# Optimization experiments

Hardware: AMD Instinct MI355X
Metric: run time of the kernel (lower is better)

Reference implementation:

```python
import jax, jax.numpy as jnp
import numpy as np

DIM = 192
HEADS = 6
HD = DIM // HEADS            # 32
RES = (32, 64, 64)           # D, H, W
WS = (4, 4, 4)               # window size
NW_TOK = WS[0] * WS[1] * WS[2]   # 64 tokens per window
L = RES[0] * RES[1] * RES[2]     # 131072
HIDDEN = 4 * DIM
B = 2


def _rel_pos_index():
    # faithful to the torch buffer construction (3D branch)
    coords = np.stack(np.meshgrid(*[np.arange(w) for w in WS], indexing='ij'))  # (3, wd, wh, ww)
    cf = coords.reshape(3, -1)                     # (3, 64)
    rel = cf[:, :, None] - cf[:, None, :]          # (3, 64, 64)
    rel = rel.transpose(1, 2, 0).astype(np.int64)  # (64, 64, 3)
    for i in range(3):
        rel[:, :, i] += WS[i] - 1
    rel[:, :, 0] *= (2 * WS[1] - 1) * (2 * WS[2] - 1)
    rel[:, :, 1] *= 2 * WS[2] - 1
    return rel.sum(-1)                             # (64, 64)


def setup_inputs() -> dict:
    key = jax.random.key(0)
    ks = jax.random.split(key, 8)
    s = 0.02
    d = {}
    d['skip'] = jax.random.normal(ks[0], (B, L, DIM), jnp.float32)
    d['x_up'] = jax.random.normal(ks[1], (B, L, DIM), jnp.float32)
    # norms
    d['g1'] = jnp.ones((DIM,), jnp.float32); d['be1'] = jnp.zeros((DIM,), jnp.float32)
    d['g2'] = jnp.ones((DIM,), jnp.float32); d['be2'] = jnp.zeros((DIM,), jnp.float32)
    # attention params
    d['Wkv'] = jax.random.normal(ks[2], (DIM, 2 * DIM), jnp.float32) * s
    d['bkv'] = jnp.zeros((2 * DIM,), jnp.float32)
    d['Wproj'] = jax.random.normal(ks[3], (DIM, DIM), jnp.float32) * s
    d['bproj'] = jnp.zeros((DIM,), jnp.float32)
    d['bias_table'] = jax.random.normal(ks[4], ((2 * WS[0] - 1) * (2 * WS[1] - 1) * (2 * WS[2] - 1), HEADS), jnp.float32) * s
    d['rel_idx'] = jnp.asarray(_rel_pos_index(), jnp.int32)
    # MLP params
    d['W1'] = jax.random.normal(ks[5], (DIM, HIDDEN), jnp.float32) * s
    d['b1'] = jnp.zeros((HIDDEN,), jnp.float32)
    d['W2'] = jax.random.normal(ks[6], (HIDDEN, DIM), jnp.float32) * s
    d['b2'] = jnp.zeros((DIM,), jnp.float32)
    return d


def _ln(x, g, b):
    mu = x.mean(-1, keepdims=True)
    var = x.var(-1, keepdims=True)
    return (x - mu) * jax.lax.rsqrt(var + 1e-5) * g + b


def _win_part(x):
    # x: (B, D, H, W, C) -> (B*nW, 64, C)
    D, H, W = RES; wd, wh, ww = WS
    x = x.reshape(B, D // wd, wd, H // wh, wh, W // ww, ww, DIM)
    x = x.transpose(0, 1, 3, 5, 2, 4, 6, 7)
    return x.reshape(-1, NW_TOK, DIM)


def _win_rev(w):
    # (B*nW, 64, C) -> (B, L, C)
    D, H, W = RES; wd, wh, ww = WS
    x = w.reshape(B, D // wd, H // wh, W // ww, wd, wh, ww, DIM)
    x = x.transpose(0, 1, 4, 2, 5, 3, 6, 7)
    return x.reshape(B, L, DIM)


def reference(skip, x_up, g1, be1, g2, be2, Wkv, bkv, Wproj, bproj,
              bias_table, rel_idx, W1, b1, W2, b2):
    shortcut = skip
    s = _ln(skip, g1, be1).reshape(B, *RES, DIM)
    u = _ln(x_up, g1, be1).reshape(B, *RES, DIM)
    sw = _win_part(s)   # kv source: (Bw, 64, C)
    uw = _win_part(u)   # q source
    Bw = sw.shape[0]
    kv = (sw @ Wkv + bkv).reshape(Bw, NW_TOK, 2, HEADS, HD)
    k = kv[:, :, 0].transpose(0, 2, 1, 3)   # (Bw, h, 64, hd)
    v = kv[:, :, 1].transpose(0, 2, 1, 3)
    q = uw.reshape(Bw, NW_TOK, HEADS, HD).transpose(0, 2, 1, 3)
    scale = HD ** -0.5
    attn = jnp.einsum('bhqd,bhkd->bhqk', q * scale, k)
    bias = bias_table[rel_idx.reshape(-1)].reshape(NW_TOK, NW_TOK, HEADS).transpose(2, 0, 1)
    attn = jax.nn.softmax(attn + bias[None], axis=-1)
    o = jnp.einsum('bhqk,bhkd->bhqd', attn, v).transpose(0, 2, 1, 3).reshape(Bw, NW_TOK, DIM)
    o = o @ Wproj + bproj
    x = shortcut + _win_rev(o)
    h = _ln(x, g2, be2)
    h = jax.nn.gelu(h @ W1 + b1, approximate=False)
    return x + (h @ W2 + b2)
```

## Files before the change

kernel.cpp:

```cpp
#include <hip/hip_runtime.h>
#include <hip/hip_bf16.h>

typedef __hip_bfloat16 bf16;
typedef short s8v __attribute__((ext_vector_type(8)));
typedef float f32x4 __attribute__((ext_vector_type(4)));

__device__ __forceinline__ float b2f(bf16 v) { return __bfloat162float(v); }
__device__ __forceinline__ bf16 f2b(float v) { return __float2bfloat16(v); }

union H8 { bf16 h[8]; s8v v; uint2 u2[2]; };

__device__ __forceinline__ float gelu_f(float v) {
    float z = fabsf(v) * 0.70710678118654752f;
    float t = 1.f / (1.f + 0.3275911f * z);
    float poly = t * (0.254829592f + t * (-0.284496736f + t * (1.421413741f +
                 t * (-1.453152027f + t * 1.061405429f))));
    float erfz = 1.f - poly * __expf(-z * z);
    erfz = copysignf(erfz, v);
    return 0.5f * v * (1.f + erfz);
}

__device__ __forceinline__ void stage_frag(const bf16* __restrict__ img, bf16* lds,
                                           int nseg, int wv, int lane) {
    for (int seg = wv; seg < nseg; seg += 4) {
        __builtin_amdgcn_global_load_lds(
            (const __attribute__((address_space(1))) void*)(img + seg * 512 + (lane << 3)),
            (__attribute__((address_space(3))) void*)(lds + seg * 512),
            16, 0, 0);
    }
}

__global__ __launch_bounds__(256) void k_prep(
    const float* __restrict__ Wkv, const float* __restrict__ Wproj,
    const float* __restrict__ W1,  const float* __restrict__ W2,
    bf16* __restrict__ ws)
{
    int t = blockIdx.x * 256 + threadIdx.x;
    if (t >= 50688) return;
    int k, n, ld;
    const float* W;
    bf16* dst;
    if (t < 9216) {
        int c = t / 1152, r = t % 1152;
        int tile = r >> 6, lane = r & 63;
        int ks = tile / 3, nt = tile % 3;
        n = c * 48 + nt * 16 + (lane & 15);
        k = ks * 32 + (lane >> 4) * 8;
        W = Wkv; ld = 384; dst = ws + t * 8;
    } else if (t < 13824) {
        int t2 = t - 9216;
        int c = t2 / 1152, r = t2 % 1152;
        int tile = r >> 6, lane = r & 63;
        int ks = tile / 3, nt = tile % 3;
        n = c * 48 + nt * 16 + (lane & 15);
        k = ks * 32 + (lane >> 4) * 8;
        W = Wproj; ld = 192; dst = ws + 73728 + t2 * 8;
    } else {
        int t3 = t - 13824;
        int c = t3 / 1536, r = t3 % 1536;
        int half = r / 768, rr = r % 768;
        int tile = rr >> 6, lane = rr & 63;
        int lr = lane & 15, g = lane >> 4;
        if (half == 0) {
            int ks = tile >> 1, nt2 = tile & 1;
            n = c * 32 + nt2 * 16 + lr; k = ks * 32 + g * 8; W = W1; ld = 768;
        } else {
            n = tile * 16 + lr; k = c * 32 + g * 8; W = W2; ld = 192;
        }
        dst = ws + 110592 + t3 * 8;
    }
    #pragma unroll
    for (int e = 0; e < 8; ++e) dst[e] = f2b(W[(k + e) * ld + n]);
}

__global__ __launch_bounds__(256, 2) void k_attn(
    const float* __restrict__ skip, const float* __restrict__ xup,
    const float* __restrict__ g1,   const float* __restrict__ be1,
    const bf16*  __restrict__ imgKv,const float* __restrict__ bkv,
    const bf16*  __restrict__ imgPr,const float* __restrict__ bproj,
    const float* __restrict__ btab, const int*  __restrict__ relidx,
    float* __restrict__ xout)
{
    __shared__ __align__(16) bf16 sK[64 * 200];
    __shared__ __align__(16) char poolRaw[36864];
    __shared__ __align__(1024) bf16 sWt[9216];

    bf16* sVt = (bf16*)poolRaw;
    bf16* sP  = (bf16*)(poolRaw + 27648);
    bf16* sO  = (bf16*)poolRaw;

    const int tid = threadIdx.x;
    const int lane = tid & 63;
    const int wv = tid >> 6;
    const int g = lane >> 4;
    const int lr = lane & 15;
    const int w = blockIdx.x;
    const int b = w >> 11;
    const int widx = w & 2047;
    const int d0 = widx >> 8, h0 = (widx >> 4) & 15, w0 = widx & 15;

    #define GROW(t) (b * 131072 + (d0 * 4 + ((t) >> 4)) * 4096 + \
                     (h0 * 4 + (((t) >> 2) & 3)) * 64 + (w0 * 4 + ((t) & 3)))

    const int myrow = wv * 16 + lr;
    const int growA = GROW(myrow) * 192;
    float4 u4[12], s4[12];
    #pragma unroll
    for (int ks = 0; ks < 6; ++ks) {
        int k0 = 32 * ks + 8 * g;
        u4[2 * ks]     = *(const float4*)(xup  + growA + k0);
        u4[2 * ks + 1] = *(const float4*)(xup  + growA + k0 + 4);
        s4[2 * ks]     = *(const float4*)(skip + growA + k0);
        s4[2 * ks + 1] = *(const float4*)(skip + growA + k0 + 4);
    }
    float su = 0, squ = 0, ss = 0, sqs = 0;
    #pragma unroll
    for (int i = 0; i < 12; ++i) {
        const float* up = &u4[i].x;
        const float* sp = &s4[i].x;
        #pragma unroll
        for (int e = 0; e < 4; ++e) {
            su += up[e]; squ += up[e] * up[e];
            ss += sp[e]; sqs += sp[e] * sp[e];
        }
    }
    su += __shfl_xor(su, 16);  su += __shfl_xor(su, 32);
    squ += __shfl_xor(squ, 16); squ += __shfl_xor(squ, 32);
    ss += __shfl_xor(ss, 16);  ss += __shfl_xor(ss, 32);
    sqs += __shfl_xor(sqs, 16); sqs += __shfl_xor(sqs, 32);
    const float inv192 = 1.f / 192.f;
    float muU = su * inv192, vU = squ * inv192 - muU * muU;
    float muS = ss * inv192, vS = sqs * inv192 - muS * muS;
    float rU = rsqrtf(vU + 1e-5f), rS = rsqrtf(vS + 1e-5f);
    const float scale = 0.17677669529663687f;

    s8v qreg[6], sreg[6];
    #pragma unroll
    for (int ks = 0; ks < 6; ++ks) {
        H8 qa, sa;
        #pragma unroll
        for (int half = 0; half < 2; ++half) {
            const float* up = &u4[2 * ks + half].x;
            const float* sp = &s4[2 * ks + half].x;
            #pragma unroll
            for (int e = 0; e < 4; ++e) {
                int k = 32 * ks + 8 * g + 4 * half + e;
                float gg = g1[k], bb = be1[k];
                qa.h[4 * half + e] = f2b(((up[e] - muU) * rU * gg + bb) * scale);
                sa.h[4 * half + e] = f2b((sp[e] - muS) * rS * gg + bb);
            }
        }
        qreg[ks] = qa.v; sreg[ks] = sa.v;
    }

    for (int nc = 0; nc < 8; ++nc) {
        __syncthreads();
        stage_frag(imgKv + nc * 9216, sWt, 18, wv, lane);
        __syncthreads();

        f32x4 acc[3];
        #pragma unroll
        for (int nt = 0; nt < 3; ++nt) acc[nt] = (f32x4){0.f, 0.f, 0.f, 0.f};
        #pragma unroll
        for (int ks = 0; ks < 6; ++ks) {
            #pragma unroll
            for (int nt = 0; nt < 3; ++nt) {
                s8v bfr = *(const s8v*)(sWt + ((ks * 3 + nt) * 64 + lane) * 8);
                acc[nt] = __builtin_amdgcn_mfma_f32_16x16x32_bf16(sreg[ks], bfr, acc[nt], 0, 0, 0);
            }
        }
        if (nc < 4) {
            #pragma unroll
            for (int nt = 0; nt < 3; ++nt) {
                int c = nc * 48 + nt * 16 + lr;
                float bias = bkv[c];
                #pragma unroll
                for (int e = 0; e < 4; ++e)
                    sK[(wv * 16 + 4 * g + e) * 200 + c] = f2b(acc[nt][e] + bias);
            }
        } else {
            #pragma unroll
            for (int nt = 0; nt < 3; ++nt) {
                int c = nc * 48 + nt * 16 + lr;
                float bias = bkv[c];
                int d = c - 192;
                H8 t4;
                #pragma unroll
                for (int e = 0; e < 4; ++e) t4.h[e] = f2b(acc[nt][e] + bias);
                *(uint2*)(sVt + d * 72 + wv * 16 + 4 * g) = t4.u2[0];
            }
        }
    }
    __syncthreads();

    int bidx[4][4];
    #pragma unroll
    for (int nt = 0; nt < 4; ++nt)
        #pragma unroll
        for (int e = 0; e < 4; ++e)
            bidx[nt][e] = relidx[(wv * 16 + 4 * g + e) * 64 + nt * 16 + lr] * 6;

    f32x4 accO[6][2];
    #pragma unroll
    for (int h = 0; h < 6; ++h)
        #pragma unroll
        for (int nt = 0; nt < 2; ++nt) accO[h][nt] = (f32x4){0.f, 0.f, 0.f, 0.f};

    #pragma unroll
    for (int h = 0; h < 6; ++h) {
        f32x4 s[4];
        #pragma unroll
        for (int nt = 0; nt < 4; ++nt) {
            s8v kf = *(const s8v*)(sK + (nt * 16 + lr) * 200 + h * 32 + 8 * g);
            s[nt] = __builtin_amdgcn_mfma_f32_16x16x32_bf16(qreg[h], kf,
                        (f32x4){0.f, 0.f, 0.f, 0.f}, 0, 0, 0);
        }
        #pragma unroll
        for (int nt = 0; nt < 4; ++nt)
            #pragma unroll
            for (int e = 0; e < 4; ++e)
                s[nt][e] += btab[bidx[nt][e] + h];
        float mx0 = fmaxf(fmaxf(s[0][0], s[1][0]), fmaxf(s[2][0], s[3][0]));
        float mx1 = fmaxf(fmaxf(s[0][1], s[1][1]), fmaxf(s[2][1], s[3][1]));
        float mx2 = fmaxf(fmaxf(s[0][2], s[1][2]), fmaxf(s[2][2], s[3][2]));
        float mx3 = fmaxf(fmaxf(s[0][3], s[1][3]), fmaxf(s[2][3], s[3][3]));
        #pragma unroll
        for (int m = 1; m <= 8; m <<= 1) {
            mx0 = fmaxf(mx0, __shfl_xor(mx0, m));
            mx1 = fmaxf(mx1, __shfl_xor(mx1, m));
            mx2 = fmaxf(mx2, __shfl_xor(mx2, m));
            mx3 = fmaxf(mx3, __shfl_xor(mx3, m));
        }
        float sm0 = 0, sm1 = 0, sm2 = 0, sm3 = 0;
        #pragma unroll
        for (int nt = 0; nt < 4; ++nt) {
            s[nt][0] = __expf(s[nt][0] - mx0); sm0 += s[nt][0];
            s[nt][1] = __expf(s[nt][1] - mx1); sm1 += s[nt][1];
            s[nt][2] = __expf(s[nt][2] - mx2); sm2 += s[nt][2];
            s[nt][3] = __expf(s[nt][3] - mx3); sm3 += s[nt][3];
        }
        #pragma unroll
        for (int m = 1; m <= 8; m <<= 1) {
            sm0 += __shfl_xor(sm0, m); sm1 += __shfl_xor(sm1, m);
            sm2 += __shfl_xor(sm2, m); sm3 += __shfl_xor(sm3, m);
        }
        float iv0 = 1.f / sm0, iv1 = 1.f / sm1, iv2 = 1.f / sm2, iv3 = 1.f / sm3;

        __syncthreads();
        #pragma unroll
        for (int nt = 0; nt < 4; ++nt) {
            int kt = nt * 16 + lr;
            sP[(wv * 16 + 4 * g + 0) * 72 + kt] = f2b(s[nt][0] * iv0);
            sP[(wv * 16 + 4 * g + 1) * 72 + kt] = f2b(s[nt][1] * iv1);
            sP[(wv * 16 + 4 * g + 2) * 72 + kt] = f2b(s[nt][2] * iv2);
            sP[(wv * 16 + 4 * g + 3) * 72 + kt] = f2b(s[nt][3] * iv3);
        }
        __syncthreads();

        s8v aP0 = *(const s8v*)(sP + (wv * 16 + lr) * 72 + 8 * g);
        s8v aP1 = *(const s8v*)(sP + (wv * 16 + lr) * 72 + 32 + 8 * g);
        #pragma unroll
        for (int nt = 0; nt < 2; ++nt) {
            const bf16* vb = sVt + (h * 32 + nt * 16 + lr) * 72;
            s8v v0 = *(const s8v*)(vb + 8 * g);
            s8v v1 = *(const s8v*)(vb + 32 + 8 * g);
            accO[h][nt] = __builtin_amdgcn_mfma_f32_16x16x32_bf16(aP0, v0, accO[h][nt], 0, 0, 0);
            accO[h][nt] = __builtin_amdgcn_mfma_f32_16x16x32_bf16(aP1, v1, accO[h][nt], 0, 0, 0);
        }
    }

    __syncthreads();
    #pragma unroll
    for (int h = 0; h < 6; ++h)
        #pragma unroll
        for (int nt = 0; nt < 2; ++nt) {
            int c = h * 32 + nt * 16 + lr;
            #pragma unroll
            for (int e = 0; e < 4; ++e)
                sO[(wv * 16 + 4 * g + e) * 200 + c] = f2b(accO[h][nt][e]);
        }
    __syncthreads();
    s8v aO[6];
    #pragma unroll
    for (int ks = 0; ks < 6; ++ks)
        aO[ks] = *(const s8v*)(sO + (wv * 16 + lr) * 200 + 32 * ks + 8 * g);

    int gq[4];
    #pragma unroll
    for (int e = 0; e < 4; ++e) gq[e] = GROW(wv * 16 + 4 * g + e) * 192;

    for (int nc = 0; nc < 4; ++nc) {
        __syncthreads();
        stage_frag(imgPr + nc * 9216, sWt, 18, wv, lane);
        __syncthreads();

        f32x4 acc[3];
        #pragma unroll
        for (int nt = 0; nt < 3; ++nt) acc[nt] = (f32x4){0.f, 0.f, 0.f, 0.f};
        #pragma unroll
        for (int ks = 0; ks < 6; ++ks) {
            #pragma unroll
            for (int nt = 0; nt < 3; ++nt) {
                s8v bfr = *(const s8v*)(sWt + ((ks * 3 + nt) * 64 + lane) * 8);
                acc[nt] = __builtin_amdgcn_mfma_f32_16x16x32_bf16(aO[ks], bfr, acc[nt], 0, 0, 0);
            }
        }
        #pragma unroll
        for (int nt = 0; nt < 3; ++nt) {
            int c = nc * 48 + nt * 16 + lr;
            float bp = bproj[c];
            #pragma unroll
            for (int e = 0; e < 4; ++e) {
                int go = gq[e] + c;
                xout[go] = acc[nt][e] + bp + skip[go];
            }
        }
    }
    #undef GROW
}

__global__ __launch_bounds__(256, 2) void k_mlp(
    float* __restrict__ xio,
    const float* __restrict__ g2, const float* __restrict__ be2,
    const bf16*  __restrict__ imgMlp,
    const float* __restrict__ b1, const float* __restrict__ b2)
{
    __shared__ __align__(1024) bf16 sW[2][12288];
    __shared__ __align__(16) bf16 sH[128 * 40];

    const int tid = threadIdx.x;
    const int lane = tid & 63;
    const int wv = tid >> 6;
    const int g = lane >> 4;
    const int lr = lane & 15;
    const int rowbase = blockIdx.x * 128;

    stage_frag(imgMlp, sW[0], 24, wv, lane);

    s8v xreg[2][6];
    #pragma unroll
    for (int mi = 0; mi < 2; ++mi) {
        const int row = rowbase + wv * 16 + mi * 64 + lr;
        float4 xa[12];
        #pragma unroll
        for (int ks = 0; ks < 6; ++ks) {
            int k0 = 32 * ks + 8 * g;
            xa[2 * ks]     = *(const float4*)(xio + row * 192 + k0);
            xa[2 * ks + 1] = *(const float4*)(xio + row * 192 + k0 + 4);
        }
        float s = 0, sq = 0;
        #pragma unroll
        for (int i = 0; i < 12; ++i) {
            const float* p = &xa[i].x;
            #pragma unroll
            for (int e = 0; e < 4; ++e) { s += p[e]; sq += p[e] * p[e]; }
        }
        s += __shfl_xor(s, 16);  s += __shfl_xor(s, 32);
        sq += __shfl_xor(sq, 16); sq += __shfl_xor(sq, 32);
        float mu = s * (1.f / 192.f), var = sq * (1.f / 192.f) - mu * mu;
        float rs = rsqrtf(var + 1e-5f);
        #pragma unroll
        for (int ks = 0; ks < 6; ++ks) {
            H8 xa8;
            #pragma unroll
            for (int half = 0; half < 2; ++half) {
                int k0 = 32 * ks + 8 * g + 4 * half;
                float4 gg = *(const float4*)(g2 + k0);
                float4 be = *(const float4*)(be2 + k0);
                const float* p = &xa[2 * ks + half].x;
                const float* gp = &gg.x;
                const float* bp = &be.x;
                #pragma unroll
                for (int e = 0; e < 4; ++e)
                    xa8.h[4 * half + e] = f2b((p[e] - mu) * rs * gp[e] + bp[e]);
            }
            xreg[mi][ks] = xa8.v;
        }
    }

    f32x4 accC[2][12];
    #pragma unroll
    for (int mi = 0; mi < 2; ++mi)
        #pragma unroll
        for (int nt = 0; nt < 12; ++nt) accC[mi][nt] = (f32x4){0.f, 0.f, 0.f, 0.f};

    for (int ch = 0; ch < 24; ++ch) {
        const int c = ch & 1;
        __syncthreads();
        if (ch < 23) stage_frag(imgMlp + (ch + 1) * 12288, sW[c ^ 1], 24, wv, lane);
        const bf16* wc = sW[c];

        f32x4 accH[2][2];
        #pragma unroll
        for (int mi = 0; mi < 2; ++mi)
            #pragma unroll
            for (int nt = 0; nt < 2; ++nt) accH[mi][nt] = (f32x4){0.f, 0.f, 0.f, 0.f};
        #pragma unroll
        for (int ks = 0; ks < 6; ++ks) {
            s8v b0  = *(const s8v*)(wc + ((ks * 2 + 0) * 64 + lane) * 8);
            s8v b1f = *(const s8v*)(wc + ((ks * 2 + 1) * 64 + lane) * 8);
            accH[0][0] = __builtin_amdgcn_mfma_f32_16x16x32_bf16(xreg[0][ks], b0,  accH[0][0], 0, 0, 0);
            accH[0][1] = __builtin_amdgcn_mfma_f32_16x16x32_bf16(xreg[0][ks], b1f, accH[0][1], 0, 0, 0);
            accH[1][0] = __builtin_amdgcn_mfma_f32_16x16x32_bf16(xreg[1][ks], b0,  accH[1][0], 0, 0, 0);
            accH[1][1] = __builtin_amdgcn_mfma_f32_16x16x32_bf16(xreg[1][ks], b1f, accH[1][1], 0, 0, 0);
        }

        #pragma unroll
        for (int mi = 0; mi < 2; ++mi)
            #pragma unroll
            for (int nt = 0; nt < 2; ++nt) {
                float bb = b1[ch * 32 + nt * 16 + lr];
                #pragma unroll
                for (int e = 0; e < 4; ++e) {
                    int row = wv * 16 + mi * 64 + g * 4 + e;
                    sH[row * 40 + nt * 16 + lr] = f2b(gelu_f(accH[mi][nt][e] + bb));
                }
            }
        __syncthreads();

        s8v aH0 = *(const s8v*)(sH + (wv * 16 + lr) * 40 + g * 8);
        s8v aH1 = *(const s8v*)(sH + (wv * 16 + 64 + lr) * 40 + g * 8);
        #pragma unroll
        for (int nt = 0; nt < 12; ++nt) {
            s8v bW = *(const s8v*)(wc + 6144 + (nt * 64 + lane) * 8);
            accC[0][nt] = __builtin_amdgcn_mfma_f32_16x16x32_bf16(aH0, bW, accC[0][nt], 0, 0, 0);
            accC[1][nt] = __builtin_amdgcn_mfma_f32_16x16x32_bf16(aH1, bW, accC[1][nt], 0, 0, 0);
        }
    }

    #pragma unroll
    for (int mi = 0; mi < 2; ++mi)
        #pragma unroll
        for (int nt = 0; nt < 12; ++nt) {
            int col = nt * 16 + lr;
            float bb = b2[col];
            #pragma unroll
            for (int e = 0; e < 4; ++e) {
                int row = rowbase + wv * 16 + mi * 64 + g * 4 + e;
                float* p = xio + row * 192 + col;
                *p = accC[mi][nt][e] + bb + *p;
            }
        }
}

extern "C" void kernel_launch(void* const* d_in, const int* in_sizes, int n_in,
                              void* d_out, int out_size, void* d_ws, size_t ws_size,
                              hipStream_t stream) {
    const float* skip   = (const float*)d_in[0];
    const float* xup    = (const float*)d_in[1];
    const float* g1     = (const float*)d_in[2];
    const float* be1    = (const float*)d_in[3];
    const float* g2     = (const float*)d_in[4];
    const float* be2    = (const float*)d_in[5];
    const float* Wkv    = (const float*)d_in[6];
    const float* bkv    = (const float*)d_in[7];
    const float* Wproj  = (const float*)d_in[8];
    const float* bproj  = (const float*)d_in[9];
    const float* btab   = (const float*)d_in[10];
    const int*  relidx  = (const int*)d_in[11];
    const float* W1     = (const float*)d_in[12];
    const float* b1     = (const float*)d_in[13];
    const float* W2     = (const float*)d_in[14];
    const float* b2     = (const float*)d_in[15];
    float* xio = (float*)d_out;
    bf16* ws = (bf16*)d_ws;

    k_prep<<<198, 256, 0, stream>>>(Wkv, Wproj, W1, W2, ws);
    k_attn<<<4096, 256, 0, stream>>>(skip, xup, g1, be1, ws, bkv,
                                     ws + 73728, bproj, btab, relidx, xio);
    k_mlp<<<2048, 256, 0, stream>>>(xio, g2, be2, ws + 110592, b1, b2);
}
```

Baseline: 612.1 us.

## Transpose MFMA operands so each wave owns its rows and drop block barriers

Swaps the A/B operands of the QK^T, PV and MLP-up MFMAs so each lane holds a whole row's values for four columns. Softmax then reduces with two cross-lane shuffles instead of four-step trees, and P, O and H fragments are written to LDS as packed 8-byte stores into rows owned only by the writing wave. That removes several __syncthreads per head and per MLP chunk. It also stages the relative-position bias table into LDS instead of reading it from global memory per element, which risks reusing the weight buffer region and relies on the per-wave LDS ownership being correct.

```diff
diff --git a/kernel.cpp b/kernel.cpp
--- a/kernel.cpp
+++ b/kernel.cpp
@@ -88,6 +88,7 @@
     bf16* sVt = (bf16*)poolRaw;
     bf16* sP  = (bf16*)(poolRaw + 27648);
     bf16* sO  = (bf16*)poolRaw;
+    float* sBt = (float*)sWt;
 
     const int tid = threadIdx.x;
     const int lane = tid & 63;
@@ -193,18 +194,20 @@
     }
     __syncthreads();
 
+    for (int i = tid; i < 2058; i += 256) sBt[i] = btab[i];
     int bidx[4][4];
     #pragma unroll
     for (int nt = 0; nt < 4; ++nt)
         #pragma unroll
         for (int e = 0; e < 4; ++e)
-            bidx[nt][e] = relidx[(wv * 16 + 4 * g + e) * 64 + nt * 16 + lr] * 6;
-
-    f32x4 accO[6][2];
+            bidx[nt][e] = relidx[(wv * 16 + lr) * 64 + nt * 16 + 4 * g + e] * 6;
+    __syncthreads();
+
+    f32x4 accOT[6][2];
     #pragma unroll
     for (int h = 0; h < 6; ++h)
         #pragma unroll
-        for (int nt = 0; nt < 2; ++nt) accO[h][nt] = (f32x4){0.f, 0.f, 0.f, 0.f};
+        for (int nt = 0; nt < 2; ++nt) accOT[h][nt] = (f32x4){0.f, 0.f, 0.f, 0.f};
 
     #pragma unroll
     for (int h = 0; h < 6; ++h) {
@@ -212,51 +215,36 @@
         #pragma unroll
         for (int nt = 0; nt < 4; ++nt) {
             s8v kf = *(const s8v*)(sK + (nt * 16 + lr) * 200 + h * 32 + 8 * g);
-            s[nt] = __builtin_amdgcn_mfma_f32_16x16x32_bf16(qreg[h], kf,
+            s[nt] = __builtin_amdgcn_mfma_f32_16x16x32_bf16(kf, qreg[h],
                         (f32x4){0.f, 0.f, 0.f, 0.f}, 0, 0, 0);
         }
         #pragma unroll
         for (int nt = 0; nt < 4; ++nt)
             #pragma unroll
             for (int e = 0; e < 4; ++e)
-                s[nt][e] += btab[bidx[nt][e] + h];
-        float mx0 = fmaxf(fmaxf(s[0][0], s[1][0]), fmaxf(s[2][0], s[3][0]));
-        float mx1 = fmaxf(fmaxf(s[0][1], s[1][1]), fmaxf(s[2][1], s[3][1]));
-        float mx2 = fmaxf(fmaxf(s[0][2], s[1][2]), fmaxf(s[2][2], s[3][2]));
-        float mx3 = fmaxf(fmaxf(s[0][3], s[1][3]), fmaxf(s[2][3], s[3][3]));
-        #pragma unroll
-        for (int m = 1; m <= 8; m <<= 1) {
-            mx0 = fmaxf(mx0, __shfl_xor(mx0, m));
-            mx1 = fmaxf(mx1, __shfl_xor(mx1, m));
-            mx2 = fmaxf(mx2, __shfl_xor(mx2, m));
-            mx3 = fmaxf(mx3, __shfl_xor(mx3, m));
-        }
-        float sm0 = 0, sm1 = 0, sm2 = 0, sm3 = 0;
+                s[nt][e] += sBt[bidx[nt][e] + h];
+        float mx = -1e30f;
+        #pragma unroll
+        for (int nt = 0; nt < 4; ++nt)
+            #pragma unroll
+            for (int e = 0; e < 4; ++e) mx = fmaxf(mx, s[nt][e]);
+        mx = fmaxf(mx, __shfl_xor(mx, 16));
+        mx = fmaxf(mx, __shfl_xor(mx, 32));
+        float sm = 0;
+        #pragma unroll
+        for (int nt = 0; nt < 4; ++nt)
+            #pragma unroll
+            for (int e = 0; e < 4; ++e) { s[nt][e] = __expf(s[nt][e] - mx); sm += s[nt][e]; }
+        sm += __shfl_xor(sm, 16);
+        sm += __shfl_xor(sm, 32);
+        float iv = 1.f / sm;
         #pragma unroll
         for (int nt = 0; nt < 4; ++nt) {
-            s[nt][0] = __expf(s[nt][0] - mx0); sm0 += s[nt][0];
-            s[nt][1] = __expf(s[nt][1] - mx1); sm1 += s[nt][1];
-            s[nt][2] = __expf(s[nt][2] - mx2); sm2 += s[nt][2];
-            s[nt][3] = __expf(s[nt][3] - mx3); sm3 += s[nt][3];
-        }
-        #pragma unroll
-        for (int m = 1; m <= 8; m <<= 1) {
-            sm0 += __shfl_xor(sm0, m); sm1 += __shfl_xor(sm1, m);
-            sm2 += __shfl_xor(sm2, m); sm3 += __shfl_xor(sm3, m);
-        }
-        float iv0 = 1.f / sm0, iv1 = 1.f / sm1, iv2 = 1.f / sm2, iv3 = 1.f / sm3;
-
-        __syncthreads();
-        #pragma unroll
-        for (int nt = 0; nt < 4; ++nt) {
-            int kt = nt * 16 + lr;
-            sP[(wv * 16 + 4 * g + 0) * 72 + kt] = f2b(s[nt][0] * iv0);
-            sP[(wv * 16 + 4 * g + 1) * 72 + kt] = f2b(s[nt][1] * iv1);
-            sP[(wv * 16 + 4 * g + 2) * 72 + kt] = f2b(s[nt][2] * iv2);
-            sP[(wv * 16 + 4 * g + 3) * 72 + kt] = f2b(s[nt][3] * iv3);
-        }
-        __syncthreads();
-
+            H8 pk;
+            #pragma unroll
+            for (int e = 0; e < 4; ++e) pk.h[e] = f2b(s[nt][e] * iv);
+            *(uint2*)(sP + (wv * 16 + lr) * 72 + nt * 16 + 4 * g) = pk.u2[0];
+        }
         s8v aP0 = *(const s8v*)(sP + (wv * 16 + lr) * 72 + 8 * g);
         s8v aP1 = *(const s8v*)(sP + (wv * 16 + lr) * 72 + 32 + 8 * g);
         #pragma unroll
@@ -264,8 +252,8 @@
             const bf16* vb = sVt + (h * 32 + nt * 16 + lr) * 72;
             s8v v0 = *(const s8v*)(vb + 8 * g);
             s8v v1 = *(const s8v*)(vb + 32 + 8 * g);
-            accO[h][nt] = __builtin_amdgcn_mfma_f32_16x16x32_bf16(aP0, v0, accO[h][nt], 0, 0, 0);
-            accO[h][nt] = __builtin_amdgcn_mfma_f32_16x16x32_bf16(aP1, v1, accO[h][nt], 0, 0, 0);
+            accOT[h][nt] = __builtin_amdgcn_mfma_f32_16x16x32_bf16(v0, aP0, accOT[h][nt], 0, 0, 0);
+            accOT[h][nt] = __builtin_amdgcn_mfma_f32_16x16x32_bf16(v1, aP1, accOT[h][nt], 0, 0, 0);
         }
     }
 
@@ -274,12 +262,11 @@
     for (int h = 0; h < 6; ++h)
         #pragma unroll
         for (int nt = 0; nt < 2; ++nt) {
-            int c = h * 32 + nt * 16 + lr;
-            #pragma unroll
-            for (int e = 0; e < 4; ++e)
-                sO[(wv * 16 + 4 * g + e) * 200 + c] = f2b(accO[h][nt][e]);
-        }
-    __syncthreads();
+            H8 pk;
+            #pragma unroll
+            for (int e = 0; e < 4; ++e) pk.h[e] = f2b(accOT[h][nt][e]);
+            *(uint2*)(sO + (wv * 16 + lr) * 200 + h * 32 + nt * 16 + 4 * g) = pk.u2[0];
+        }
     s8v aO[6];
     #pragma unroll
     for (int ks = 0; ks < 6; ++ks)
@@ -390,33 +377,33 @@
         if (ch < 23) stage_frag(imgMlp + (ch + 1) * 12288, sW[c ^ 1], 24, wv, lane);
         const bf16* wc = sW[c];
 
-        f32x4 accH[2][2];
+        f32x4 accHT[2][2];
         #pragma unroll
         for (int mi = 0; mi < 2; ++mi)
             #pragma unroll
-            for (int nt = 0; nt < 2; ++nt) accH[mi][nt] = (f32x4){0.f, 0.f, 0.f, 0.f};
+            for (int nt = 0; nt < 2; ++nt) accHT[mi][nt] = (f32x4){0.f, 0.f, 0.f, 0.f};
         #pragma unroll
         for (int ks = 0; ks < 6; ++ks) {
-            s8v b0  = *(const s8v*)(wc + ((ks * 2 + 0) * 64 + lane) * 8);
-            s8v b1f = *(const s8v*)(wc + ((ks * 2 + 1) * 64 + lane) * 8);
-            accH[0][0] = __builtin_amdgcn_mfma_f32_16x16x32_bf16(xreg[0][ks], b0,  accH[0][0], 0, 0, 0);
-            accH[0][1] = __builtin_amdgcn_mfma_f32_16x16x32_bf16(xreg[0][ks], b1f, accH[0][1], 0, 0, 0);
-            accH[1][0] = __builtin_amdgcn_mfma_f32_16x16x32_bf16(xreg[1][ks], b0,  accH[1][0], 0, 0, 0);
-            accH[1][1] = __builtin_amdgcn_mfma_f32_16x16x32_bf16(xreg[1][ks], b1f, accH[1][1], 0, 0, 0);
+            s8v w0 = *(const s8v*)(wc + ((ks * 2 + 0) * 64 + lane) * 8);
+            s8v w1 = *(const s8v*)(wc + ((ks * 2 + 1) * 64 + lane) * 8);
+            accHT[0][0] = __builtin_amdgcn_mfma_f32_16x16x32_bf16(w0, xreg[0][ks], accHT[0][0], 0, 0, 0);
+            accHT[0][1] = __builtin_amdgcn_mfma_f32_16x16x32_bf16(w1, xreg[0][ks], accHT[0][1], 0, 0, 0);
+            accHT[1][0] = __builtin_amdgcn_mfma_f32_16x16x32_bf16(w0, xreg[1][ks], accHT[1][0], 0, 0, 0);
+            accHT[1][1] = __builtin_amdgcn_mfma_f32_16x16x32_bf16(w1, xreg[1][ks], accHT[1][1], 0, 0, 0);
         }
 
         #pragma unroll
         for (int mi = 0; mi < 2; ++mi)
             #pragma unroll
-            for (int nt = 0; nt < 2; ++nt) {
-                float bb = b1[ch * 32 + nt * 16 + lr];
+            for (int nt2 = 0; nt2 < 2; ++nt2) {
+                float4 b1v = *(const float4*)(b1 + ch * 32 + nt2 * 16 + 4 * g);
+                const float* bp = &b1v.x;
+                H8 pk;
                 #pragma unroll
-                for (int e = 0; e < 4; ++e) {
-                    int row = wv * 16 + mi * 64 + g * 4 + e;
-                    sH[row * 40 + nt * 16 + lr] = f2b(gelu_f(accH[mi][nt][e] + bb));
-                }
-            }
-        __syncthreads();
+                for (int e = 0; e < 4; ++e)
+                    pk.h[e] = f2b(gelu_f(accHT[mi][nt2][e] + bp[e]));
+                *(uint2*)(sH + (wv * 16 + mi * 64 + lr) * 40 + nt2 * 16 + 4 * g) = pk.u2[0];
+            }
 
         s8v aH0 = *(const s8v*)(sH + (wv * 16 + lr) * 40 + g * 8);
         s8v aH1 = *(const s8v*)(sH + (wv * 16 + 64 + lr) * 40 + g * 8);
```

After: 586.6 us. 1.04x faster.
